# Optimization experiments

Measured on AMD Instinct MI355X. Metric: run time of the kernel, lower is better.

Reference implementation:

```python
import jax, jax.numpy as jnp
import numpy as np

B, S, DM, DA, H, F = 4, 1024, 512, 512, 8, 16
D = DA // H  # per-head depth = 64


def setup_inputs() -> dict:
    key = jax.random.key(0)
    ks = jax.random.split(key, 10)
    w = lambda i, shape: jax.random.normal(ks[i], shape, jnp.float32) * 0.02
    return {
        "q": jax.random.normal(ks[0], (B, S, DM), jnp.float32),
        "k": jax.random.normal(ks[1], (B, S, DM), jnp.float32),
        "v": jax.random.normal(ks[2], (B, S, DM), jnp.float32),
        "xdiff": jax.random.normal(ks[3], (B, S, S, F), jnp.float32),
        "Wq": w(4, (DM, DA)), "bq": jnp.zeros((DA,), jnp.float32),
        "Wk": w(5, (DM, DA)), "bk": jnp.zeros((DA,), jnp.float32),
        "Wv": w(6, (DM, DA)), "bv": jnp.zeros((DA,), jnp.float32),
        "Wx": w(7, (DA, H * F)), "bx": jnp.zeros((H * F,), jnp.float32),
        "Wo": w(8, (DA, DM)), "bo": jnp.zeros((DM,), jnp.float32),
    }


def reference(q, k, v, xdiff, Wq, bq, Wk, bk, Wv, bv, Wx, bx, Wo, bo):
    b, s, _ = q.shape
    qp = q @ Wq + bq                      # [B,S,DA]
    kp = k @ Wk + bk                      # [B,S,DA]
    vp = v @ Wv + bv                      # [B,S,DA]
    x = qp @ Wx + bx                      # [B,S,H*F]  (note: wx applied to projected q)
    qh = qp.reshape(b, s, H, D).transpose(0, 2, 1, 3)   # [B,H,S,D]
    kh = kp.reshape(b, s, H, D).transpose(0, 2, 1, 3)
    vh = vp.reshape(b, s, H, D).transpose(0, 2, 1, 3)
    xh = x.reshape(b, s, H, F)                           # [B,S,H,F]
    # xdiff relative bias: matmul(xdiff, x^T) then transpose -> [B,H,Sq,Sk]
    x_logits = jnp.einsum('bqkf,bqhf->bhqk', xdiff, xh)
    scaled_x_logits = 2.0 * x_logits / jnp.sqrt(jnp.float32(F))
    logits = jnp.einsum('bhqd,bhkd->bhqk', qh, kh) / jnp.sqrt(jnp.float32(D))
    logits = logits + scaled_x_logits
    attn = jax.nn.softmax(logits, axis=-1)               # [B,H,Sq,Sk]
    out = jnp.einsum('bhqk,bhkd->bhqd', attn, vh)        # [B,H,S,D]
    out = out.transpose(0, 2, 1, 3).reshape(b, s, DA)    # [B,S,DA]
    output = out @ Wo + bo                               # [B,S,DM]
    return (output, attn)
```

## Files before the change

### kernel.cpp

```cpp
#include <hip/hip_runtime.h>

typedef unsigned int uint;
typedef unsigned short ushort;
typedef __attribute__((ext_vector_type(4))) float f32x4;
typedef __attribute__((ext_vector_type(8))) __bf16 bf16x8;

#define MFMA16(a,b,c) __builtin_amdgcn_mfma_f32_16x16x32_bf16(a,b,c,0,0,0)

__device__ __forceinline__ ushort f2bf(float f){
  uint u = __float_as_uint(f);
  u += 0x7fffu + ((u>>16)&1u);
  return (ushort)(u>>16);
}
__device__ __forceinline__ float bf2f(ushort s){ return __uint_as_float(((uint)s)<<16); }
__device__ __forceinline__ uint packbf2(float a, float b){ return (uint)f2bf(a) | ((uint)f2bf(b)<<16); }

__global__ __launch_bounds__(256) void wt_kernel(const float* __restrict__ W,
    ushort* __restrict__ WT, int K, int N){
  int e = blockIdx.x*256 + threadIdx.x;
  if (e >= K*N) return;
  int n = e % N, k = e / N;
  WT[(size_t)n*K + k] = f2bf(W[(size_t)k*N + n]);
}

template<bool A_F32, bool OUT_F32>
__global__ __launch_bounds__(256) void gemm_bt(const void* __restrict__ Av,
    const ushort* __restrict__ Bt, const float* __restrict__ bias,
    void* __restrict__ Cv, int M, int N, int K){
  __shared__ ushort As[64*48];
  __shared__ ushort Bs[64*48];
  const int tid = threadIdx.x;
  const int m0 = blockIdx.y<<6, n0 = blockIdx.x<<6;
  const int wave = tid>>6, lane = tid&63;
  const int wr = wave&1, wc = wave>>1;
  const int fl = lane&15, quad = lane>>4;
  f32x4 acc[2][2] = {};
  const int srow = tid>>2, sk = (tid&3)<<3;
  for (int k0 = 0; k0 < K; k0 += 32){
    if (A_F32){
      const float* A = (const float*)Av;
      const float4* pa = reinterpret_cast<const float4*>(A + (size_t)(m0+srow)*K + k0 + sk);
      float4 v0 = pa[0], v1 = pa[1];
      uint4 pk = make_uint4(packbf2(v0.x,v0.y), packbf2(v0.z,v0.w),
                            packbf2(v1.x,v1.y), packbf2(v1.z,v1.w));
      *reinterpret_cast<uint4*>(&As[srow*48 + sk]) = pk;
    } else {
      const ushort* A = (const ushort*)Av;
      *reinterpret_cast<uint4*>(&As[srow*48 + sk]) =
          *reinterpret_cast<const uint4*>(A + (size_t)(m0+srow)*K + k0 + sk);
    }
    *reinterpret_cast<uint4*>(&Bs[srow*48 + sk]) =
        *reinterpret_cast<const uint4*>(Bt + (size_t)(n0+srow)*K + k0 + sk);
    __syncthreads();
    bf16x8 a0 = *reinterpret_cast<const bf16x8*>(&As[(32*wr      + fl)*48 + quad*8]);
    bf16x8 a1 = *reinterpret_cast<const bf16x8*>(&As[(32*wr + 16 + fl)*48 + quad*8]);
    bf16x8 b0 = *reinterpret_cast<const bf16x8*>(&Bs[(32*wc      + fl)*48 + quad*8]);
    bf16x8 b1 = *reinterpret_cast<const bf16x8*>(&Bs[(32*wc + 16 + fl)*48 + quad*8]);
    acc[0][0] = MFMA16(a0,b0,acc[0][0]);
    acc[0][1] = MFMA16(a0,b1,acc[0][1]);
    acc[1][0] = MFMA16(a1,b0,acc[1][0]);
    acc[1][1] = MFMA16(a1,b1,acc[1][1]);
    __syncthreads();
  }
  #pragma unroll
  for (int t=0;t<2;++t)
  #pragma unroll
  for (int u=0;u<2;++u){
    #pragma unroll
    for (int r=0;r<4;++r){
      int row = m0 + 32*wr + 16*t + quad*4 + r;
      int col = n0 + 32*wc + 16*u + fl;
      float vv = acc[t][u][r] + bias[col];
      if (OUT_F32) ((float*)Cv)[(size_t)row*N + col] = vv;
      else         ((ushort*)Cv)[(size_t)row*N + col] = f2bf(vv);
    }
  }
}

__global__ __launch_bounds__(256) void vtrans(const ushort* __restrict__ vp,
    ushort* __restrict__ vT){
  __shared__ ushort tile[64*72];
  const int bh = blockIdx.y;
  const int b = bh>>3, h = bh&7;
  const int k0 = blockIdx.x<<6;
  const int tid = threadIdx.x;
  #pragma unroll
  for (int i=0;i<2;++i){
    int c = tid + (i<<8);
    int row = c>>3, ch = (c&7)<<3;
    uint4 v = *reinterpret_cast<const uint4*>(
        vp + ((size_t)(b*1024 + k0 + row)<<9) + (h<<6) + ch);
    *reinterpret_cast<uint4*>(&tile[row*72 + ch]) = v;
  }
  __syncthreads();
  #pragma unroll
  for (int i=0;i<2;++i){
    int c = tid + (i<<8);
    int d = c>>3, sc = (c&7)<<3;
    ushort t0 = tile[(sc+0)*72 + d], t1 = tile[(sc+1)*72 + d];
    ushort t2 = tile[(sc+2)*72 + d], t3 = tile[(sc+3)*72 + d];
    ushort t4 = tile[(sc+4)*72 + d], t5 = tile[(sc+5)*72 + d];
    ushort t6 = tile[(sc+6)*72 + d], t7 = tile[(sc+7)*72 + d];
    uint4 pk = make_uint4((uint)t0|((uint)t1<<16), (uint)t2|((uint)t3<<16),
                          (uint)t4|((uint)t5<<16), (uint)t6|((uint)t7<<16));
    *reinterpret_cast<uint4*>(vT + (((size_t)bh<<6) + d)*1024 + k0 + sc) = pk;
  }
}

__global__ __launch_bounds__(256) void xl_kernel(const float* __restrict__ xdiff,
    const ushort* __restrict__ xb, ushort* __restrict__ xl){
  const int bq = blockIdx.x;
  const int b = bq>>10, q = bq&1023;
  __shared__ float sx[8][16];
  const int tid = threadIdx.x;
  if (tid < 128) sx[tid>>4][tid&15] = bf2f(xb[(size_t)bq*128 + tid]);
  __syncthreads();
  const float* xd = xdiff + (size_t)bq*16384;
  #pragma unroll
  for (int i=0;i<4;++i){
    int k = tid + (i<<8);
    const float4* p = reinterpret_cast<const float4*>(xd + (size_t)k*16);
    float4 v0 = p[0], v1 = p[1], v2 = p[2], v3 = p[3];
    #pragma unroll
    for (int h=0; h<8; ++h){
      const float4* s = reinterpret_cast<const float4*>(&sx[h][0]);
      float4 s0=s[0], s1=s[1], s2=s[2], s3=s[3];
      float a = v0.x*s0.x + v0.y*s0.y + v0.z*s0.z + v0.w*s0.w
              + v1.x*s1.x + v1.y*s1.y + v1.z*s1.z + v1.w*s1.w
              + v2.x*s2.x + v2.y*s2.y + v2.z*s2.z + v2.w*s2.w
              + v3.x*s3.x + v3.y*s3.y + v3.z*s3.z + v3.w*s3.w;
      xl[(((size_t)((b<<3)+h)<<10) + q)*1024 + k] = f2bf(0.5f*a);
    }
  }
}

__global__ __launch_bounds__(256) void attn_kernel(const ushort* __restrict__ qp,
    const ushort* __restrict__ kp, const ushort* __restrict__ vT,
    const ushort* __restrict__ xl, float* __restrict__ attn, ushort* __restrict__ outc){
  __shared__ ushort s_p[32*1024];
  const int qt = blockIdx.x, h = blockIdx.y, b = blockIdx.z;
  const int q0 = qt<<5;
  const int tid = threadIdx.x, lane = tid&63, wave = tid>>6;
  const int wr = wave&1, wc = wave>>1;
  const int fl = lane&15, quad = lane>>4;
  const size_t bS = (size_t)b<<10;
  const int bh = (b<<3) + h;

  bf16x8 aq[2];
  #pragma unroll
  for (int s=0;s<2;++s)
    aq[s] = *reinterpret_cast<const bf16x8*>(
        qp + ((bS + q0 + (wr<<4) + fl)<<9) + (h<<6) + (s<<5) + (quad<<3));

  for (int kt=0; kt<16; ++kt){
    f32x4 acc0 = {}, acc1 = {};
    #pragma unroll
    for (int s=0;s<2;++s){
      const ushort* kbase = kp + ((bS + (kt<<6) + (wc<<5) + fl)<<9) + (h<<6) + (s<<5) + (quad<<3);
      bf16x8 b0 = *reinterpret_cast<const bf16x8*>(kbase);
      bf16x8 b1 = *reinterpret_cast<const bf16x8*>(kbase + (16<<9));
      acc0 = MFMA16(aq[s], b0, acc0);
      acc1 = MFMA16(aq[s], b1, acc1);
    }
    #pragma unroll
    for (int u=0;u<2;++u){
      f32x4 a = u ? acc1 : acc0;
      #pragma unroll
      for (int r=0;r<4;++r){
        int row = (wr<<4) + (quad<<2) + r;
        int col = (kt<<6) + (wc<<5) + (u<<4) + fl;
        int chunk = (col>>3) ^ (row&7);
        s_p[(row<<10) + (chunk<<3) + (col&7)] = f2bf(a[r]*0.125f);
      }
    }
  }
  __syncthreads();

  const int r = tid>>3, seg = tid&7, swz = r&7;
  const ushort* xrow = xl + (((size_t)bh<<10) + q0 + r)*1024;
  float* arow = attn + (((size_t)bh<<10) + q0 + r)*1024;
  float mx = -3.0e38f;
  for (int cc=0; cc<16; ++cc){
    int chunk = (seg<<4) + cc;
    uint4 lv = *reinterpret_cast<uint4*>(&s_p[(r<<10) + ((chunk^swz)<<3)]);
    uint4 xv = *reinterpret_cast<const uint4*>(xrow + (chunk<<3));
    float f0 = bf2f(lv.x&0xffff)+bf2f(xv.x&0xffff), f1 = bf2f(lv.x>>16)+bf2f(xv.x>>16);
    float f2 = bf2f(lv.y&0xffff)+bf2f(xv.y&0xffff), f3 = bf2f(lv.y>>16)+bf2f(xv.y>>16);
    float f4 = bf2f(lv.z&0xffff)+bf2f(xv.z&0xffff), f5 = bf2f(lv.z>>16)+bf2f(xv.z>>16);
    float f6 = bf2f(lv.w&0xffff)+bf2f(xv.w&0xffff), f7 = bf2f(lv.w>>16)+bf2f(xv.w>>16);
    mx = fmaxf(mx, fmaxf(fmaxf(fmaxf(f0,f1),fmaxf(f2,f3)), fmaxf(fmaxf(f4,f5),fmaxf(f6,f7))));
    uint4 pk = make_uint4(packbf2(f0,f1), packbf2(f2,f3), packbf2(f4,f5), packbf2(f6,f7));
    *reinterpret_cast<uint4*>(&s_p[(r<<10) + ((chunk^swz)<<3)]) = pk;
  }
  #pragma unroll
  for (int d=1; d<8; d<<=1) mx = fmaxf(mx, __shfl_xor(mx, d));
  float sum = 0.f;
  for (int cc=0; cc<16; ++cc){
    int chunk = (seg<<4) + cc;
    uint4 lv = *reinterpret_cast<uint4*>(&s_p[(r<<10) + ((chunk^swz)<<3)]);
    ushort u0 = f2bf(__expf(bf2f(lv.x&0xffff)-mx)), u1 = f2bf(__expf(bf2f(lv.x>>16)-mx));
    ushort u2 = f2bf(__expf(bf2f(lv.y&0xffff)-mx)), u3 = f2bf(__expf(bf2f(lv.y>>16)-mx));
    ushort u4 = f2bf(__expf(bf2f(lv.z&0xffff)-mx)), u5 = f2bf(__expf(bf2f(lv.z>>16)-mx));
    ushort u6 = f2bf(__expf(bf2f(lv.w&0xffff)-mx)), u7 = f2bf(__expf(bf2f(lv.w>>16)-mx));
    sum += bf2f(u0)+bf2f(u1)+bf2f(u2)+bf2f(u3)+bf2f(u4)+bf2f(u5)+bf2f(u6)+bf2f(u7);
    uint4 pk = make_uint4((uint)u0|((uint)u1<<16), (uint)u2|((uint)u3<<16),
                          (uint)u4|((uint)u5<<16), (uint)u6|((uint)u7<<16));
    *reinterpret_cast<uint4*>(&s_p[(r<<10) + ((chunk^swz)<<3)]) = pk;
  }
  #pragma unroll
  for (int d=1; d<8; d<<=1) sum += __shfl_xor(sum, d);
  float inv = 1.f/sum;
  for (int cc=0; cc<16; ++cc){
    int chunk = (seg<<4) + cc;
    uint4 lv = *reinterpret_cast<uint4*>(&s_p[(r<<10) + ((chunk^swz)<<3)]);
    float o0 = bf2f(lv.x&0xffff)*inv, o1 = bf2f(lv.x>>16)*inv;
    float o2 = bf2f(lv.y&0xffff)*inv, o3 = bf2f(lv.y>>16)*inv;
    float o4 = bf2f(lv.z&0xffff)*inv, o5 = bf2f(lv.z>>16)*inv;
    float o6 = bf2f(lv.w&0xffff)*inv, o7 = bf2f(lv.w>>16)*inv;
    *reinterpret_cast<float4*>(arow + (chunk<<3))     = make_float4(o0,o1,o2,o3);
    *reinterpret_cast<float4*>(arow + (chunk<<3) + 4) = make_float4(o4,o5,o6,o7);
    uint4 pk = make_uint4(packbf2(o0,o1), packbf2(o2,o3), packbf2(o4,o5), packbf2(o6,o7));
    *reinterpret_cast<uint4*>(&s_p[(r<<10) + ((chunk^swz)<<3)]) = pk;
  }
  __syncthreads();

  f32x4 o0 = {}, o1 = {};
  const int ar = (wr<<4) + fl;
  const int aswz = ar & 7;
  for (int kt=0; kt<16; ++kt){
    #pragma unroll
    for (int s=0;s<2;++s){
      int chunk = (kt<<3) + (s<<2) + quad;
      bf16x8 af = *reinterpret_cast<const bf16x8*>(&s_p[(ar<<10) + ((chunk^aswz)<<3)]);
      const ushort* vbase = vT + (((size_t)bh<<6) + (wc<<5) + fl)*1024 + (kt<<6) + (s<<5) + (quad<<3);
      bf16x8 b0 = *reinterpret_cast<const bf16x8*>(vbase);
      bf16x8 b1 = *reinterpret_cast<const bf16x8*>(vbase + (16<<10));
      o0 = MFMA16(af, b0, o0);
      o1 = MFMA16(af, b1, o1);
    }
  }
  #pragma unroll
  for (int u=0;u<2;++u){
    f32x4 a = u ? o1 : o0;
    #pragma unroll
    for (int r4=0;r4<4;++r4){
      int row = (wr<<4) + (quad<<2) + r4;
      int col = (wc<<5) + (u<<4) + fl;
      outc[((bS + q0 + row)<<9) + (h<<6) + col] = f2bf(a[r4]);
    }
  }
}

extern "C" void kernel_launch(void* const* d_in, const int* in_sizes, int n_in,
                              void* d_out, int out_size, void* d_ws, size_t ws_size,
                              hipStream_t stream){
  (void)in_sizes; (void)n_in; (void)out_size; (void)ws_size;
  const float* q  = (const float*)d_in[0];
  const float* k  = (const float*)d_in[1];
  const float* v  = (const float*)d_in[2];
  const float* xd = (const float*)d_in[3];
  const float* Wq = (const float*)d_in[4];  const float* bq = (const float*)d_in[5];
  const float* Wk = (const float*)d_in[6];  const float* bk = (const float*)d_in[7];
  const float* Wv = (const float*)d_in[8];  const float* bv = (const float*)d_in[9];
  const float* Wx = (const float*)d_in[10]; const float* bx = (const float*)d_in[11];
  const float* Wo = (const float*)d_in[12]; const float* bo = (const float*)d_in[13];
  char* ws = (char*)d_ws;
  const size_t MB = 1u<<20;
  ushort* qp  = (ushort*)(ws);
  ushort* kp  = (ushort*)(ws + 4*MB);
  ushort* vp  = (ushort*)(ws + 8*MB);
  ushort* vT  = (ushort*)(ws + 12*MB);
  ushort* xb  = (ushort*)(ws + 16*MB);
  ushort* xl  = (ushort*)(ws + 17*MB);
  ushort* oc  = (ushort*)(ws + 81*MB);
  ushort* WqT = (ushort*)(ws + 85*MB);
  ushort* WkT = (ushort*)(ws + 85*MB + 1*524288);
  ushort* WvT = (ushort*)(ws + 85*MB + 2*524288);
  ushort* WoT = (ushort*)(ws + 85*MB + 3*524288);
  ushort* WxT = (ushort*)(ws + 85*MB + 4*524288);
  float* out0 = (float*)d_out;
  float* attn = (float*)d_out + 2097152;

  wt_kernel<<<1024, 256, 0, stream>>>(Wq, WqT, 512, 512);
  wt_kernel<<<1024, 256, 0, stream>>>(Wk, WkT, 512, 512);
  wt_kernel<<<1024, 256, 0, stream>>>(Wv, WvT, 512, 512);
  wt_kernel<<<1024, 256, 0, stream>>>(Wo, WoT, 512, 512);
  wt_kernel<<< 256, 256, 0, stream>>>(Wx, WxT, 512, 128);

  gemm_bt<true,false><<<dim3(8,64), 256, 0, stream>>>(q, WqT, bq, qp, 4096, 512, 512);
  gemm_bt<true,false><<<dim3(8,64), 256, 0, stream>>>(k, WkT, bk, kp, 4096, 512, 512);
  gemm_bt<true,false><<<dim3(8,64), 256, 0, stream>>>(v, WvT, bv, vp, 4096, 512, 512);
  gemm_bt<false,false><<<dim3(2,64), 256, 0, stream>>>(qp, WxT, bx, xb, 4096, 128, 512);

  vtrans<<<dim3(16,32), 256, 0, stream>>>(vp, vT);
  xl_kernel<<<4096, 256, 0, stream>>>(xd, xb, xl);
  attn_kernel<<<dim3(32,8,4), 256, 0, stream>>>(qp, kp, vT, xl, attn, oc);
  gemm_bt<false,true><<<dim3(8,64), 256, 0, stream>>>(oc, WoT, bo, out0, 4096, 512, 512);
}
```

Before: 656.3 us.

## Tile weight transpose via shared memory and double attention block threads

Weight conversion to transposed bf16 now uses a 64x64 shared-memory tile, so global reads and writes are coalesced and vectorized instead of strided per element. The attention kernel moves from 256 to 512 threads per block. Each wave now computes one 16-column MFMA tile instead of two, and each row's softmax is split across 16 threads instead of 8. The shared-memory swizzle changes to match the new access pattern. This adds parallelism per block for the memory-bound softmax and attn write phase, at the cost of more threads competing for the same 64KB of LDS per block.

```diff
diff --git a/kernel.cpp b/kernel.cpp
--- a/kernel.cpp
+++ b/kernel.cpp
@@ -17,10 +17,36 @@
 
 __global__ __launch_bounds__(256) void wt_kernel(const float* __restrict__ W,
     ushort* __restrict__ WT, int K, int N){
-  int e = blockIdx.x*256 + threadIdx.x;
-  if (e >= K*N) return;
-  int n = e % N, k = e / N;
-  WT[(size_t)n*K + k] = f2bf(W[(size_t)k*N + n]);
+  __shared__ uint tile[64*65];
+  const int k0 = blockIdx.y<<6, n0 = blockIdx.x<<6;
+  const int tid = threadIdx.x;
+  {
+    const int row = tid>>4, c4 = (tid&15)<<2;
+    #pragma unroll
+    for (int i=0;i<4;++i){
+      int r = row + (i<<4);
+      float4 v = *reinterpret_cast<const float4*>(W + (size_t)(k0+r)*N + n0 + c4);
+      tile[r*65 + c4    ] = f2bf(v.x);
+      tile[r*65 + c4 + 1] = f2bf(v.y);
+      tile[r*65 + c4 + 2] = f2bf(v.z);
+      tile[r*65 + c4 + 3] = f2bf(v.w);
+    }
+  }
+  __syncthreads();
+  {
+    const int n = tid>>3, k8 = (tid&7)<<3;
+    #pragma unroll
+    for (int j=0;j<2;++j){
+      int nn = n + (j<<5);
+      ushort t0=(ushort)tile[(k8+0)*65+nn], t1=(ushort)tile[(k8+1)*65+nn];
+      ushort t2=(ushort)tile[(k8+2)*65+nn], t3=(ushort)tile[(k8+3)*65+nn];
+      ushort t4=(ushort)tile[(k8+4)*65+nn], t5=(ushort)tile[(k8+5)*65+nn];
+      ushort t6=(ushort)tile[(k8+6)*65+nn], t7=(ushort)tile[(k8+7)*65+nn];
+      uint4 pk = make_uint4((uint)t0|((uint)t1<<16), (uint)t2|((uint)t3<<16),
+                            (uint)t4|((uint)t5<<16), (uint)t6|((uint)t7<<16));
+      *reinterpret_cast<uint4*>(WT + (size_t)(n0+nn)*K + k0 + k8) = pk;
+    }
+  }
 }
 
 template<bool A_F32, bool OUT_F32>
@@ -134,7 +160,7 @@
   }
 }
 
-__global__ __launch_bounds__(256) void attn_kernel(const ushort* __restrict__ qp,
+__global__ __launch_bounds__(512) void attn_kernel(const ushort* __restrict__ qp,
     const ushort* __restrict__ kp, const ushort* __restrict__ vT,
     const ushort* __restrict__ xl, float* __restrict__ attn, ushort* __restrict__ outc){
   __shared__ ushort s_p[32*1024];
@@ -153,35 +179,29 @@
         qp + ((bS + q0 + (wr<<4) + fl)<<9) + (h<<6) + (s<<5) + (quad<<3));
 
   for (int kt=0; kt<16; ++kt){
-    f32x4 acc0 = {}, acc1 = {};
+    f32x4 acc = {};
     #pragma unroll
     for (int s=0;s<2;++s){
-      const ushort* kbase = kp + ((bS + (kt<<6) + (wc<<5) + fl)<<9) + (h<<6) + (s<<5) + (quad<<3);
-      bf16x8 b0 = *reinterpret_cast<const bf16x8*>(kbase);
-      bf16x8 b1 = *reinterpret_cast<const bf16x8*>(kbase + (16<<9));
-      acc0 = MFMA16(aq[s], b0, acc0);
-      acc1 = MFMA16(aq[s], b1, acc1);
-    }
-    #pragma unroll
-    for (int u=0;u<2;++u){
-      f32x4 a = u ? acc1 : acc0;
-      #pragma unroll
-      for (int r=0;r<4;++r){
-        int row = (wr<<4) + (quad<<2) + r;
-        int col = (kt<<6) + (wc<<5) + (u<<4) + fl;
-        int chunk = (col>>3) ^ (row&7);
-        s_p[(row<<10) + (chunk<<3) + (col&7)] = f2bf(a[r]*0.125f);
-      }
-    }
-  }
-  __syncthreads();
-
-  const int r = tid>>3, seg = tid&7, swz = r&7;
+      bf16x8 bf = *reinterpret_cast<const bf16x8*>(
+          kp + ((bS + (kt<<6) + (wc<<4) + fl)<<9) + (h<<6) + (s<<5) + (quad<<3));
+      acc = MFMA16(aq[s], bf, acc);
+    }
+    #pragma unroll
+    for (int r=0;r<4;++r){
+      int row = (wr<<4) + (quad<<2) + r;
+      int col = (kt<<6) + (wc<<4) + fl;
+      int chunk = (col>>3) ^ ((row>>1)&7);
+      s_p[(row<<10) + (chunk<<3) + (col&7)] = f2bf(acc[r]*0.125f);
+    }
+  }
+  __syncthreads();
+
+  const int r = tid>>4, seg = tid&15, swz = (r>>1)&7;
   const ushort* xrow = xl + (((size_t)bh<<10) + q0 + r)*1024;
   float* arow = attn + (((size_t)bh<<10) + q0 + r)*1024;
   float mx = -3.0e38f;
-  for (int cc=0; cc<16; ++cc){
-    int chunk = (seg<<4) + cc;
+  for (int cc=0; cc<8; ++cc){
+    int chunk = (cc<<4) + seg;
     uint4 lv = *reinterpret_cast<uint4*>(&s_p[(r<<10) + ((chunk^swz)<<3)]);
     uint4 xv = *reinterpret_cast<const uint4*>(xrow + (chunk<<3));
     float f0 = bf2f(lv.x&0xffff)+bf2f(xv.x&0xffff), f1 = bf2f(lv.x>>16)+bf2f(xv.x>>16);
@@ -193,10 +213,10 @@
     *reinterpret_cast<uint4*>(&s_p[(r<<10) + ((chunk^swz)<<3)]) = pk;
   }
   #pragma unroll
-  for (int d=1; d<8; d<<=1) mx = fmaxf(mx, __shfl_xor(mx, d));
+  for (int d=1; d<16; d<<=1) mx = fmaxf(mx, __shfl_xor(mx, d));
   float sum = 0.f;
-  for (int cc=0; cc<16; ++cc){
-    int chunk = (seg<<4) + cc;
+  for (int cc=0; cc<8; ++cc){
+    int chunk = (cc<<4) + seg;
     uint4 lv = *reinterpret_cast<uint4*>(&s_p[(r<<10) + ((chunk^swz)<<3)]);
     ushort u0 = f2bf(__expf(bf2f(lv.x&0xffff)-mx)), u1 = f2bf(__expf(bf2f(lv.x>>16)-mx));
     ushort u2 = f2bf(__expf(bf2f(lv.y&0xffff)-mx)), u3 = f2bf(__expf(bf2f(lv.y>>16)-mx));
@@ -208,10 +228,10 @@
     *reinterpret_cast<uint4*>(&s_p[(r<<10) + ((chunk^swz)<<3)]) = pk;
   }
   #pragma unroll
-  for (int d=1; d<8; d<<=1) sum += __shfl_xor(sum, d);
+  for (int d=1; d<16; d<<=1) sum += __shfl_xor(sum, d);
   float inv = 1.f/sum;
-  for (int cc=0; cc<16; ++cc){
-    int chunk = (seg<<4) + cc;
+  for (int cc=0; cc<8; ++cc){
+    int chunk = (cc<<4) + seg;
     uint4 lv = *reinterpret_cast<uint4*>(&s_p[(r<<10) + ((chunk^swz)<<3)]);
     float o0 = bf2f(lv.x&0xffff)*inv, o1 = bf2f(lv.x>>16)*inv;
     float o2 = bf2f(lv.y&0xffff)*inv, o3 = bf2f(lv.y>>16)*inv;
@@ -224,30 +244,24 @@
   }
   __syncthreads();
 
-  f32x4 o0 = {}, o1 = {};
+  f32x4 o = {};
   const int ar = (wr<<4) + fl;
-  const int aswz = ar & 7;
+  const int aswz = (ar>>1)&7;
   for (int kt=0; kt<16; ++kt){
     #pragma unroll
     for (int s=0;s<2;++s){
       int chunk = (kt<<3) + (s<<2) + quad;
       bf16x8 af = *reinterpret_cast<const bf16x8*>(&s_p[(ar<<10) + ((chunk^aswz)<<3)]);
-      const ushort* vbase = vT + (((size_t)bh<<6) + (wc<<5) + fl)*1024 + (kt<<6) + (s<<5) + (quad<<3);
-      bf16x8 b0 = *reinterpret_cast<const bf16x8*>(vbase);
-      bf16x8 b1 = *reinterpret_cast<const bf16x8*>(vbase + (16<<10));
-      o0 = MFMA16(af, b0, o0);
-      o1 = MFMA16(af, b1, o1);
-    }
-  }
-  #pragma unroll
-  for (int u=0;u<2;++u){
-    f32x4 a = u ? o1 : o0;
-    #pragma unroll
-    for (int r4=0;r4<4;++r4){
-      int row = (wr<<4) + (quad<<2) + r4;
-      int col = (wc<<5) + (u<<4) + fl;
-      outc[((bS + q0 + row)<<9) + (h<<6) + col] = f2bf(a[r4]);
-    }
+      bf16x8 bf = *reinterpret_cast<const bf16x8*>(
+          vT + (((size_t)bh<<6) + (wc<<4) + fl)*1024 + (kt<<6) + (s<<5) + (quad<<3));
+      o = MFMA16(af, bf, o);
+    }
+  }
+  #pragma unroll
+  for (int r4=0;r4<4;++r4){
+    int row = (wr<<4) + (quad<<2) + r4;
+    int col = (wc<<4) + fl;
+    outc[((bS + q0 + row)<<9) + (h<<6) + col] = f2bf(o[r4]);
   }
 }
 
@@ -281,11 +295,11 @@
   float* out0 = (float*)d_out;
   float* attn = (float*)d_out + 2097152;
 
-  wt_kernel<<<1024, 256, 0, stream>>>(Wq, WqT, 512, 512);
-  wt_kernel<<<1024, 256, 0, stream>>>(Wk, WkT, 512, 512);
-  wt_kernel<<<1024, 256, 0, stream>>>(Wv, WvT, 512, 512);
-  wt_kernel<<<1024, 256, 0, stream>>>(Wo, WoT, 512, 512);
-  wt_kernel<<< 256, 256, 0, stream>>>(Wx, WxT, 512, 128);
+  wt_kernel<<<dim3(8,8), 256, 0, stream>>>(Wq, WqT, 512, 512);
+  wt_kernel<<<dim3(8,8), 256, 0, stream>>>(Wk, WkT, 512, 512);
+  wt_kernel<<<dim3(8,8), 256, 0, stream>>>(Wv, WvT, 512, 512);
+  wt_kernel<<<dim3(8,8), 256, 0, stream>>>(Wo, WoT, 512, 512);
+  wt_kernel<<<dim3(2,8), 256, 0, stream>>>(Wx, WxT, 512, 128);
 
   gemm_bt<true,false><<<dim3(8,64), 256, 0, stream>>>(q, WqT, bq, qp, 4096, 512, 512);
   gemm_bt<true,false><<<dim3(8,64), 256, 0, stream>>>(k, WkT, bk, kp, 4096, 512, 512);
@@ -294,6 +308,6 @@
 
   vtrans<<<dim3(16,32), 256, 0, stream>>>(vp, vT);
   xl_kernel<<<4096, 256, 0, stream>>>(xd, xb, xl);
-  attn_kernel<<<dim3(32,8,4), 256, 0, stream>>>(qp, kp, vT, xl, attn, oc);
+  attn_kernel<<<dim3(32,8,4), 512, 0, stream>>>(qp, kp, vT, xl, attn, oc);
   gemm_bt<false,true><<<dim3(8,64), 256, 0, stream>>>(oc, WoT, bo, out0, 4096, 512, 512);
 }
```

Result: faster. 611.8 us (-6.8%).
